# Optimization experiments

Measured on AMD Instinct MI355X. Metric: run time of the kernel, lower is better.

The kernel has to match this reference:

```python
import jax, jax.numpy as jnp
import numpy as np

NEG_INF = -1e5  # module default neg_inf


def setup_inputs() -> dict:
    key = jax.random.key(0)
    k1, k2 = jax.random.split(key)
    B, T, V, U = 64, 1000, 512, 256
    log_posteriors = jax.random.normal(k1, (B, T, V), dtype=jnp.float32)
    lens = jnp.ones((B,), dtype=jnp.float32)
    phns = jax.random.randint(k2, (B, U), 0, V)
    phn_lens = jnp.ones((B,), dtype=jnp.float32)
    return {"log_posteriors": log_posteriors, "lens": lens, "phns": phns, "phn_lens": phn_lens}


def _forward_scores(log_posteriors, lens, phns, phn_lens):
    B, T, V = log_posteriors.shape
    U = phns.shape[1]
    lens_abs = jnp.round(lens * T).astype(jnp.int32)
    phn_lens_abs = jnp.round(phn_lens * U).astype(jnp.int32)

    # --- pi: all initial mass on first phoneme ---
    pi = jnp.full((B, U), NEG_INF, dtype=jnp.float32).at[:, 0].set(0.0)

    # --- transition log-probs: self-loop + advance-by-one, length-masked, row log_softmax ---
    base = jnp.eye(U, dtype=jnp.float32) + jnp.eye(U, k=1, dtype=jnp.float32)  # (U,U)
    m = jnp.arange(U)[None, :] < phn_lens_abs[:, None]  # (B,U) valid-phoneme mask
    m2 = m[:, :, None] & m[:, None, :]  # (B,U,U)
    masked = base[None, :, :] * m2.astype(jnp.float32)
    logits = jnp.where(masked == 1.0, 1.0, -jnp.inf)
    trans = jax.nn.log_softmax(logits, axis=2)
    # nan (all -inf rows) and -inf -> neg_inf, as in the torch module
    trans = jnp.where(jnp.isnan(trans) | jnp.isinf(trans), NEG_INF, trans)  # (B,U,U)

    # --- emissions rearranged to phoneme-sequence order: (B, U, T) as (T, B, U) scan seq ---
    mask_t = jnp.arange(T)[None, :] < lens_abs[:, None]  # (B,T)
    ep = jnp.where(mask_t[:, :, None], log_posteriors, NEG_INF)
    idx = jnp.broadcast_to(phns[:, None, :], (B, T, U))
    gathered = jnp.take_along_axis(ep, idx, axis=2)  # (B,T,U)
    emiss = jnp.where(m[:, None, :], gathered, NEG_INF)  # (B,T,U)
    emiss_seq = jnp.swapaxes(emiss, 0, 1)  # (T,B,U)

    # --- forward DP: alpha[t,i] = logsumexp_j(trans[j,i] + alpha[t-1,j]) + emiss[t,i] ---
    transT = jnp.swapaxes(trans, 1, 2)  # (B, to, from)
    alpha0 = pi + emiss_seq[0]  # (B,U), unmasked as in torch (masked entries ~2*neg_inf anyway)

    def step(alpha, e_t):
        x = jax.nn.logsumexp(transT + alpha[:, None, :], axis=2)  # batch_log_matvecmul
        alpha_new = jnp.where(m, x + e_t, NEG_INF)
        return alpha_new, None

    alphaT, _ = jax.lax.scan(step, alpha0, emiss_seq[1:])
    return jax.nn.logsumexp(alphaT, axis=1)  # (B,) log-likelihoods


def reference(log_posteriors, lens, phns, phn_lens):
    return _forward_scores(log_posteriors, lens, phns, phn_lens)
```

## Files before the change

### kernel.cpp

```cpp
#include <hip/hip_runtime.h>
#include <math.h>

constexpr int Bc = 64;
constexpr int Tc = 1000;
constexpr int Vc = 512;
constexpr int Uc = 256;
constexpr int CH = 50;
constexpr int NCH = Tc / CH;
constexpr int PW = 7;
constexpr int SLOTS = 4;

constexpr int GW = 2;
constexpr int GNR = 10;
constexpr int GROWS = GW * GNR;
constexpr int GBLK = Tc / GROWS;

constexpr int FPC = CH * Uc * 2 / 1024;

#define NEG_INF_F (-100000.0f)
#define LOG2E_F 1.44269504088896340736f
#define LN2_F 0.69314718055994530942f
#define DEAD_F (-1.0e9f)
#define EBIAS 30

#define WAITVM(n) __builtin_amdgcn_s_waitcnt(((n) & 15) | (((n) >> 4) << 14) | 0x0f70)

__device__ __forceinline__ float fexp2(float x) {
#if __has_builtin(__builtin_amdgcn_exp2f)
    return __builtin_amdgcn_exp2f(x);
#else
    return __expf(x * LN2_F);
#endif
}
__device__ __forceinline__ float flog2(float x) {
#if __has_builtin(__builtin_amdgcn_logf)
    return __builtin_amdgcn_logf(x);
#else
    return __logf(x) * LOG2E_F;
#endif
}

__device__ __forceinline__ float l2add(float x, float y) {
    float m = fmaxf(x, y);
    float p = fexp2(-fabsf(x - y));
    return m + flog2(1.0f + p);
}

__device__ __forceinline__ float waveshr1(float x, float lane0val) {
    return __int_as_float(__builtin_amdgcn_update_dpp(
        __float_as_int(lane0val), __float_as_int(x),
        0x138 , 0xF, 0xF, false));
}
__device__ __forceinline__ int waveshr1_i(int x) {
    return __builtin_amdgcn_update_dpp(x, x, 0x138, 0xF, 0xF, false);
}

__device__ __forceinline__ float4 unbf(uint2 u) {
    float4 f;
    f.x = __uint_as_float(u.x << 16);
    f.y = __uint_as_float(u.x & 0xffff0000u);
    f.z = __uint_as_float(u.y << 16);
    f.w = __uint_as_float(u.y & 0xffff0000u);
    return f;
}
__device__ __forceinline__ unsigned int bfpack(float a, float b) {
    unsigned int xa = __float_as_uint(a), xb = __float_as_uint(b);
    xa = (xa + 0x7fffu + ((xa >> 16) & 1u)) >> 16;
    xb = (xb + 0x7fffu + ((xb >> 16) & 1u)) & 0xffff0000u;
    return xa | xb;
}

__device__ __forceinline__ void hmm_step_f32(float rr[4], const float4 ev,
                                             float sc_d) {
    float nb0 = waveshr1(rr[3], 0.0f) * sc_d;
    float s0 = rr[0] + nb0;
    float s1 = rr[1] + rr[0];
    float s2 = rr[2] + rr[1];
    float s3 = rr[3] + rr[2];
    rr[0] = s0 * ev.x;
    rr[1] = s1 * ev.y;
    rr[2] = s2 * ev.z;
    rr[3] = s3 * ev.w;
}

__device__ __forceinline__ void hmm_step(float rr[4], const float4 ev) {
    float nb0 = waveshr1(rr[3], DEAD_F);
    float e[4] = {ev.x, ev.y, ev.z, ev.w};
    float nb[4] = {nb0, rr[0], rr[1], rr[2]};
#pragma unroll
    for (int c = 0; c < 4; ++c) {
        float x = rr[c], y = nb[c];
        float m = fmaxf(x, y);
        float p = fexp2(-fabsf(x - y));
        float me = m + e[c];
        rr[c] = me + flog2(1.0f + p);
    }
}

template <int AUX>
__device__ __forceinline__ void dma16x(const void* gsrc, void* lds, int lane) {
    typedef const __attribute__((address_space(1))) unsigned int* gp_t;
    typedef __attribute__((address_space(3))) unsigned int* lp_t;
    __builtin_amdgcn_global_load_lds((gp_t)((const char*)gsrc + 16 * lane),
                                     (lp_t)lds, 16, 0, AUX);
}
__device__ __forceinline__ void dma16(const void* g, void* l, int lane) {
    dma16x<0>(g, l, lane);
}
__device__ __forceinline__ void dma16nt(const void* g, void* l, int lane) {
    dma16x<2>(g, l, lane);
}

__global__ __launch_bounds__(128, 2) void gather_kernel(
    const float* __restrict__ lp, const float* __restrict__ lens,
    const int* __restrict__ phns, const float* __restrict__ phn_lens,
    unsigned short* __restrict__ el) {
    __shared__ float stage[GW][GNR][Vc];
    const int b = blockIdx.x;
    const int t0 = blockIdx.y * GROWS;
    const int tid = threadIdx.x;
    const int wave = tid >> 6;
    const int lane = tid & 63;
    const int Tv = (int)rintf(lens[b] * (float)Tc);
    const int Uv = (int)rintf(phn_lens[b] * (float)Uc);
    const float* lpb = lp + (size_t)b * Tc * Vc;
    unsigned short* elb = el + ((size_t)b * Tc + t0) * Uc;

    int col[4];
    float off[4];
    bool pv[4];
    int4 cc = *(const int4*)(phns + (size_t)b * Uc + 4 * lane);
    int c4[4] = {cc.x, cc.y, cc.z, cc.w};
#pragma unroll
    for (int c = 0; c < 4; ++c) {
        int v = c4[c];
        v = v < 0 ? 0 : (v > Vc - 1 ? Vc - 1 : v);
        col[c] = v;
        int i = 4 * lane + c;
        pv[c] = (i < Uv);
        off[c] = (i == Uv - 1) ? 0.0f : -1.0f;
    }

    float* stw = &stage[wave][0][0];
#pragma unroll
    for (int j = 0; j < GNR; ++j) {
        int r = wave + j * GW;
        const float* gsrc = lpb + (size_t)(t0 + r) * Vc;
        float* st = stw + j * Vc;
        dma16nt(gsrc, st, lane);
        dma16nt(gsrc + 256, st + 256, lane);
    }

    auto do_rows = [&](int j0) {
#pragma unroll
        for (int j = j0; j < j0 + GNR / 2; ++j) {
            int r = wave + j * GW;
            const bool tv = (t0 + r) < Tv;
            const float* st = stw + j * Vc;
            float ev[4];
#pragma unroll
            for (int c = 0; c < 4; ++c) {
                float e = st[col[c]];
                ev[c] = (pv[c] && tv) ? fexp2(fmaf(e, LOG2E_F, off[c])) : 0.0f;
            }
            uint2 pk;
            pk.x = bfpack(ev[0], ev[1]);
            pk.y = bfpack(ev[2], ev[3]);
            *(uint2*)((char*)elb + (size_t)r * Uc * 2 + 8 * lane) = pk;
        }
    };

    WAITVM(10);
    do_rows(0);
    WAITVM(0);
    do_rows(GNR / 2);
}

__global__ __launch_bounds__(128, 1) void scan_kernel(
    const unsigned short* __restrict__ el, const float* __restrict__ phn_lens,
    float* __restrict__ out) {
    __shared__ unsigned short ebuf[4][CH][Uc];
    const int b = blockIdx.x;
    const int tid = threadIdx.x;
    const int wave = tid >> 6;
    const int lane = tid & 63;
    const int Uv = (int)rintf(phn_lens[b] * (float)Uc);
    const char* eb = (const char*)(el + (size_t)b * Tc * Uc);
    float rr[4];
    int e = 0;
    float sc_d = 1.0f;

    auto fill = [&](int k) {
        const char* src = eb + (size_t)k * CH * Uc * 2;
        char* dst = (char*)&ebuf[k & 3][0][0];
#pragma unroll
        for (int i = 0; i < FPC; ++i)
            dma16(src + i * 1024, dst + i * 1024, lane);
    };

    auto renorm = [&]() {
        float m = fmaxf(fmaxf(rr[0], rr[1]), fmaxf(rr[2], rr[3]));
        int ep_old = waveshr1_i(e);
        bool nz = (m > 0.0f);
        int ik = ((__float_as_int(m) >> 23) & 255) - 127 - EBIAS;
        ik = ik < -96 ? -96 : (ik > 96 ? 96 : ik);
        const float sc = __int_as_float((127 - ik) << 23);
        rr[0] *= sc; rr[1] *= sc; rr[2] *= sc; rr[3] *= sc;
        e = nz ? (e + ik) : ep_old;
        int ep = waveshr1_i(e);
        int d = ep - e;
        int dc = d < -126 ? -126 : (d > 127 ? 127 : d);
        float sd = __int_as_float((127 + dc) << 23);
        sc_d = (d < -126) ? 0.0f : sd;
    };

    auto consume = [&](int k) {
        const uint2* base = (const uint2*)&ebuf[k & 3][0][0] + lane;
        int r = 0;
        if (k == 0) {
            float4 e0 = unbf(base[0]);
            float ea[4] = {e0.x, e0.y, e0.z, e0.w};
#pragma unroll
            for (int c = 0; c < 4; ++c)
                rr[c] = (4 * lane + c == 0) ? ea[c] : 0.0f;
            r = 1;
        }
        uint2 q0, q1, q2, q3;
        if (r + 0 < CH) q0 = base[(r + 0) * 64];
        if (r + 1 < CH) q1 = base[(r + 1) * 64];
        if (r + 2 < CH) q2 = base[(r + 2) * 64];
        if (r + 3 < CH) q3 = base[(r + 3) * 64];
        while (r + 4 <= CH) {
            uint2 e0 = q0, e1 = q1, e2v = q2, e3 = q3;
            if (r + 4 < CH) q0 = base[(r + 4) * 64];
            if (r + 5 < CH) q1 = base[(r + 5) * 64];
            if (r + 6 < CH) q2 = base[(r + 6) * 64];
            if (r + 7 < CH) q3 = base[(r + 7) * 64];
            hmm_step_f32(rr, unbf(e0), sc_d);
            hmm_step_f32(rr, unbf(e1), sc_d);
            hmm_step_f32(rr, unbf(e2v), sc_d);
            hmm_step_f32(rr, unbf(e3), sc_d);
            renorm();
            r += 4;
        }
        bool tail = false;
        if (r + 0 < CH) { hmm_step_f32(rr, unbf(q0), sc_d); tail = true; }
        if (r + 1 < CH) { hmm_step_f32(rr, unbf(q1), sc_d); }
        if (r + 2 < CH) { hmm_step_f32(rr, unbf(q2), sc_d); }
        if (tail) renorm();
    };

    WAITVM(0);
    if (wave == 0) {
        fill(0); fill(2);
    } else {
        fill(1); fill(3);
    }

    for (int k = 0; k < NCH; ++k) {
        if ((k & 1) == 0) {
            if (wave == 0) {
                if (k < NCH - 2) WAITVM(FPC);
                else WAITVM(0);
                consume(k);
                if (k + 4 < NCH) fill(k + 4);
            }
        } else {
            if (wave == 1) {
                if (k < NCH - 2) WAITVM(FPC);
                else WAITVM(0);
            }
            __syncthreads();
            if (wave == 0) consume(k);
            __syncthreads();
            if (wave == 1 && k + 4 < NCH) fill(k + 4);
        }
    }

    if (wave != 0) return;
    float a = 0.0f;
#pragma unroll
    for (int c = 0; c < 4; ++c)
        a += rr[c] * ((4 * lane + c == Uv - 1) ? 1.0f : 2.0f);
    float v = (a > 0.0f) ? (flog2(a) + (float)e) : -1.0e30f;
#pragma unroll
    for (int o = 32; o >= 1; o >>= 1) {
        float t = __shfl_xor(v, o, 64);
        v = l2add(v, t);
    }
    if (lane == 0) out[b] = v * LN2_F;
}

__global__ __launch_bounds__(512, 1) void fused_hmm_kernel(
    const float* __restrict__ lp, const float* __restrict__ lens,
    const int* __restrict__ phns, const float* __restrict__ phn_lens,
    float* __restrict__ out) {
    __shared__ float ebuf[2][CH][Uc];
    __shared__ float stage[PW][SLOTS][Vc];
    const int b = blockIdx.x;
    const int tid = threadIdx.x;
    const int wave = tid >> 6;
    const int lane = tid & 63;
    const int Tv = (int)rintf(lens[b] * (float)Tc);
    const int Uv = (int)rintf(phn_lens[b] * (float)Uc);
    const float* lpb = lp + (size_t)b * Tc * Vc;

    int col[4];
    float off[4];
    bool pv[4];
    float rr[4];

    if (wave > 0) {
        int4 cc = *(const int4*)(phns + (size_t)b * Uc + 4 * lane);
        int c4[4] = {cc.x, cc.y, cc.z, cc.w};
#pragma unroll
        for (int c = 0; c < 4; ++c) {
            int v = c4[c];
            v = v < 0 ? 0 : (v > Vc - 1 ? Vc - 1 : v);
            col[c] = v;
            int i = 4 * lane + c;
            pv[c] = (i < Uv);
            off[c] = (i == Uv - 1) ? 0.0f : -1.0f;
        }
    }

    auto fill = [&](int k) {
        float* dst = &ebuf[k & 1][0][0];
        const int tb = k * CH;
        const int r0 = wave - 1;
        float* stw = &stage[wave - 1][0][0];
#pragma unroll
        for (int half = 0; half < 2; ++half) {
#pragma unroll
            for (int jj = 0; jj < SLOTS; ++jj) {
                int r = r0 + (half * SLOTS + jj) * PW;
                if (r < CH) {
                    const float* gsrc = lpb + (size_t)(tb + r) * Vc;
                    float* st = stw + jj * Vc;
                    dma16(gsrc, st, lane);
                    dma16(gsrc + 256, st + 256, lane);
                }
            }
            WAITVM(0);
#pragma unroll
            for (int jj = 0; jj < SLOTS; ++jj) {
                int r = r0 + (half * SLOTS + jj) * PW;
                if (r < CH) {
                    const bool tv = (tb + r) < Tv;
                    const float* st = stw + jj * Vc;
                    float ev[4];
#pragma unroll
                    for (int c = 0; c < 4; ++c) {
                        float e = st[col[c]];
                        ev[c] = (pv[c] && tv) ? fmaf(e, LOG2E_F, off[c])
                                              : (NEG_INF_F * LOG2E_F + off[c]);
                    }
                    *(float4*)(dst + r * Uc + 4 * lane) =
                        make_float4(ev[0], ev[1], ev[2], ev[3]);
                }
            }
        }
    };

    auto consume = [&](int k) {
        const float4* base = (const float4*)&ebuf[k & 1][0][0] + lane;
        int r = 0;
        if (k == 0) {
            float4 e0 = base[0];
            float ea[4] = {e0.x, e0.y, e0.z, e0.w};
#pragma unroll
            for (int c = 0; c < 4; ++c)
                rr[c] = ((4 * lane + c == 0) ? 0.0f : DEAD_F) + ea[c];
            r = 1;
        }
        float4 q0, q1, q2, q3;
        if (r + 0 < CH) q0 = base[(r + 0) * 64];
        if (r + 1 < CH) q1 = base[(r + 1) * 64];
        if (r + 2 < CH) q2 = base[(r + 2) * 64];
        if (r + 3 < CH) q3 = base[(r + 3) * 64];
        while (r + 4 <= CH) {
            float4 e0 = q0, e1 = q1, e2 = q2, e3 = q3;
            if (r + 4 < CH) q0 = base[(r + 4) * 64];
            if (r + 5 < CH) q1 = base[(r + 5) * 64];
            if (r + 6 < CH) q2 = base[(r + 6) * 64];
            if (r + 7 < CH) q3 = base[(r + 7) * 64];
            hmm_step(rr, e0);
            hmm_step(rr, e1);
            hmm_step(rr, e2);
            hmm_step(rr, e3);
            r += 4;
        }
        if (r + 0 < CH) hmm_step(rr, q0);
        if (r + 1 < CH) hmm_step(rr, q1);
        if (r + 2 < CH) hmm_step(rr, q2);
    };

    if (wave > 0) fill(0);
    __syncthreads();
    for (int k = 0; k < NCH; ++k) {
        if (wave > 0) {
            if (k + 1 < NCH) fill(k + 1);
        } else {
            consume(k);
        }
        __syncthreads();
    }

    if (wave == 0) {
        float a[4];
#pragma unroll
        for (int c = 0; c < 4; ++c)
            a[c] = rr[c] + ((4 * lane + c == Uv - 1) ? 0.0f : 1.0f);
        float r2 = l2add(l2add(a[0], a[1]), l2add(a[2], a[3]));
#pragma unroll
        for (int o = 32; o >= 1; o >>= 1) {
            float t = __shfl_xor(r2, o, 64);
            r2 = l2add(r2, t);
        }
        if (lane == 0) out[b] = r2 * LN2_F;
    }
}

extern "C" void kernel_launch(void* const* d_in, const int* in_sizes, int n_in,
                              void* d_out, int out_size, void* d_ws, size_t ws_size,
                              hipStream_t stream) {
    const float* lp = (const float*)d_in[0];
    const float* lens = (const float*)d_in[1];
    const int* phns = (const int*)d_in[2];
    const float* phn_lens = (const float*)d_in[3];
    float* out = (float*)d_out;
    (void)in_sizes; (void)n_in; (void)out_size;

    const size_t need = (size_t)Bc * Tc * Uc * 2;
    if (d_ws != nullptr && ws_size >= need) {
        unsigned short* el = (unsigned short*)d_ws;
        gather_kernel<<<dim3(Bc, GBLK), 128, 0, stream>>>(lp, lens, phns,
                                                          phn_lens, el);
        scan_kernel<<<Bc, 128, 0, stream>>>(el, phn_lens, out);
    } else {
        fused_hmm_kernel<<<Bc, 512, 0, stream>>>(lp, lens, phns, phn_lens, out);
    }
}
```

Measured before the change: 241.0 us.

## Fuse pairs of HMM steps into one two-step transfer with precomputed coefficients

Combines two consecutive forward-DP time steps into a single update. It precomputes the two-step banded transition coefficients (self, advance-one, advance-two) from the two emission rows. This halves the number of dependent cross-lane shift and FMA chains on the serial recurrence and renormalizes after every 8 rows instead of 4. In exchange it does more independent multiplies per step, and the longer interval between renormalizations risks float overflow or underflow.

```diff
diff --git a/kernel.cpp b/kernel.cpp
--- a/kernel.cpp
+++ b/kernel.cpp
@@ -214,40 +214,54 @@
         sc_d = (d < -126) ? 0.0f : sd;
     };
 
+    auto pairstep = [&](const float4 E1, const float4 E2) {
+        float e1m0 = waveshr1(E1.w, 0.0f);
+        float a0 = E2.x * E1.x, a1 = E2.y * E1.y;
+        float a2 = E2.z * E1.z, a3 = E2.w * E1.w;
+        float b0 = E2.x * (E1.x + e1m0);
+        float b1 = E2.y * (E1.y + E1.x);
+        float b2 = E2.z * (E1.z + E1.y);
+        float b3 = E2.w * (E1.w + E1.z);
+        float c0 = E2.x * e1m0;
+        float c1 = E2.y * E1.x;
+        float c2 = E2.z * E1.y;
+        float c3 = E2.w * E1.z;
+        float rl3 = waveshr1(rr[3], 0.0f) * sc_d;
+        float rl2 = waveshr1(rr[2], 0.0f) * sc_d;
+        float n0 = fmaf(a0, rr[0], fmaf(b0, rl3, c0 * rl2));
+        float n1 = fmaf(a1, rr[1], fmaf(b1, rr[0], c1 * rl3));
+        float n2 = fmaf(a2, rr[2], fmaf(b2, rr[1], c2 * rr[0]));
+        float n3 = fmaf(a3, rr[3], fmaf(b3, rr[2], c3 * rr[1]));
+        rr[0] = n0; rr[1] = n1; rr[2] = n2; rr[3] = n3;
+    };
+
     auto consume = [&](int k) {
         const uint2* base = (const uint2*)&ebuf[k & 3][0][0] + lane;
-        int r = 0;
+        int r0row = 0;
         if (k == 0) {
             float4 e0 = unbf(base[0]);
             float ea[4] = {e0.x, e0.y, e0.z, e0.w};
 #pragma unroll
             for (int c = 0; c < 4; ++c)
                 rr[c] = (4 * lane + c == 0) ? ea[c] : 0.0f;
-            r = 1;
-        }
-        uint2 q0, q1, q2, q3;
-        if (r + 0 < CH) q0 = base[(r + 0) * 64];
-        if (r + 1 < CH) q1 = base[(r + 1) * 64];
-        if (r + 2 < CH) q2 = base[(r + 2) * 64];
-        if (r + 3 < CH) q3 = base[(r + 3) * 64];
-        while (r + 4 <= CH) {
-            uint2 e0 = q0, e1 = q1, e2v = q2, e3 = q3;
-            if (r + 4 < CH) q0 = base[(r + 4) * 64];
-            if (r + 5 < CH) q1 = base[(r + 5) * 64];
-            if (r + 6 < CH) q2 = base[(r + 6) * 64];
-            if (r + 7 < CH) q3 = base[(r + 7) * 64];
-            hmm_step_f32(rr, unbf(e0), sc_d);
-            hmm_step_f32(rr, unbf(e1), sc_d);
-            hmm_step_f32(rr, unbf(e2v), sc_d);
-            hmm_step_f32(rr, unbf(e3), sc_d);
+            hmm_step_f32(rr, unbf(base[64]), sc_d);
+            r0row = 2;
+        }
+        auto group4 = [&](int r) {
+            uint2 w[8];
+#pragma unroll
+            for (int i = 0; i < 8; ++i) w[i] = base[(r + i) * 64];
+#pragma unroll
+            for (int p = 0; p < 4; ++p)
+                pairstep(unbf(w[2 * p]), unbf(w[2 * p + 1]));
             renorm();
-            r += 4;
-        }
-        bool tail = false;
-        if (r + 0 < CH) { hmm_step_f32(rr, unbf(q0), sc_d); tail = true; }
-        if (r + 1 < CH) { hmm_step_f32(rr, unbf(q1), sc_d); }
-        if (r + 2 < CH) { hmm_step_f32(rr, unbf(q2), sc_d); }
-        if (tail) renorm();
+        };
+#pragma unroll
+        for (int g = 0; g < 6; ++g) group4(r0row + g * 8);
+        if (r0row == 0) {
+            pairstep(unbf(base[48 * 64]), unbf(base[49 * 64]));
+            renorm();
+        }
     };
 
     WAITVM(0);
```

Result: no change. 240.1 us, median of 2 (-0.4%).
